# Performance work log

Measured on AMD Instinct MI355X. Metric: run time of the kernel, lower is better.

The kernel has to match this reference:

```python
import jax, jax.numpy as jnp
import numpy as np

D_MODEL = 1024
N_HEADS = 16
HEAD_DIM = D_MODEL // N_HEADS
ROPE_BASE = 10000.0


def setup_inputs() -> dict:
    key = jax.random.key(0)
    ks = jax.random.split(key, 5)
    B, S = 2, 2048
    x = jax.random.normal(ks[0], (B, S, D_MODEL), dtype=jnp.float32)
    scale = 1.0 / np.sqrt(D_MODEL)
    Wq = jax.random.normal(ks[1], (D_MODEL, D_MODEL), dtype=jnp.float32) * scale
    Wk = jax.random.normal(ks[2], (D_MODEL, D_MODEL), dtype=jnp.float32) * scale
    Wv = jax.random.normal(ks[3], (D_MODEL, D_MODEL), dtype=jnp.float32) * scale
    Wo = jax.random.normal(ks[4], (D_MODEL, D_MODEL), dtype=jnp.float32) * scale
    return {"x": x, "Wq": Wq, "Wk": Wk, "Wv": Wv, "Wo": Wo}


def _rope_cos_sin(seq_len, dtype):
    # inv_freq over half the head dim, duplicated (cat[freqs, freqs])
    inv_freq = 1.0 / (ROPE_BASE ** (jnp.arange(0, HEAD_DIM, 2, dtype=jnp.float32) / HEAD_DIM))
    t = jnp.arange(seq_len, dtype=jnp.float32)
    freqs = jnp.outer(t, inv_freq)                 # [S, HD/2]
    emb = jnp.concatenate([freqs, freqs], axis=-1)  # [S, HD]
    return jnp.cos(emb).astype(dtype), jnp.sin(emb).astype(dtype)


def _rotate_half(v):
    v1, v2 = jnp.split(v, 2, axis=-1)
    return jnp.concatenate([-v2, v1], axis=-1)


def reference(x, Wq, Wk, Wv, Wo):
    B, S, _ = x.shape
    # torch Linear: y = x @ W.T  (weights stored [out, in])
    def proj(W):
        y = jnp.einsum('bsd,ed->bse', x, W)
        return y.reshape(B, S, N_HEADS, HEAD_DIM).transpose(0, 2, 1, 3)  # [B,H,S,HD]
    q, k, v = proj(Wq), proj(Wk), proj(Wv)

    cos, sin = _rope_cos_sin(S, x.dtype)  # [S, HD]
    cos = cos[None, None]                 # [1,1,S,HD]
    sin = sin[None, None]
    q = q * cos + _rotate_half(q) * sin
    k = k * cos + _rotate_half(k) * sin

    scale = 1.0 / np.sqrt(HEAD_DIM)
    scores = jnp.einsum('bhqd,bhkd->bhqk', q, k) * scale  # [B,H,S,S]
    causal = jnp.triu(jnp.ones((S, S), dtype=bool), k=1)
    scores = jnp.where(causal, jnp.finfo(scores.dtype).min, scores)
    attn = jax.nn.softmax(scores, axis=-1)
    out = jnp.einsum('bhqk,bhkd->bhqd', attn, v)          # [B,H,S,HD]
    out = out.transpose(0, 2, 1, 3).reshape(B, S, D_MODEL)
    return jnp.einsum('bsd,ed->bse', out, Wo)
```

## Files before the change

### kernel.cpp

```cpp
#include <hip/hip_runtime.h>

typedef unsigned short u16;
typedef __attribute__((ext_vector_type(8))) short short8;
typedef __attribute__((ext_vector_type(4))) float floatx4;

#define D_MODEL 1024
#define NHEADS 16
#define HD 64
#define BATCH 2
#define SEQ 2048
#define MROWS (BATCH * SEQ)

static __device__ __forceinline__ u16 f2bf(float f) {
  unsigned int u = __float_as_uint(f);
  u += 0x7fffu + ((u >> 16) & 1u);
  return (u16)(u >> 16);
}

__global__ void cvt_all(const float* __restrict__ x, const float* __restrict__ wq,
                        const float* __restrict__ wk, const float* __restrict__ wv,
                        const float* __restrict__ wo, u16* __restrict__ xb,
                        u16* __restrict__ wqkvb, u16* __restrict__ wob) {
  const int i = blockIdx.x * 256 + threadIdx.x;
  const int chunk = i >> 18;
  const float* src;
  u16* dst;
  int loc;
  switch (chunk) {
    case 0: case 1: case 2: case 3: src = x;  dst = xb;              loc = i;              break;
    case 4:                          src = wq; dst = wqkvb;           loc = i - (4 << 18); break;
    case 5:                          src = wk; dst = wqkvb + 1048576; loc = i - (5 << 18); break;
    case 6:                          src = wv; dst = wqkvb + 2097152; loc = i - (6 << 18); break;
    default:                         src = wo; dst = wob;             loc = i - (7 << 18); break;
  }
  const float4 v = ((const float4*)src)[loc];
  ushort4 o;
  o.x = f2bf(v.x); o.y = f2bf(v.y); o.z = f2bf(v.z); o.w = f2bf(v.w);
  ((ushort4*)dst)[loc] = o;
}

__global__ __launch_bounds__(256) void gemm_qkv(
    const u16* __restrict__ A, const u16* __restrict__ B,
    u16* __restrict__ qb, u16* __restrict__ kb, u16* __restrict__ vb, int K) {
  __shared__ u16 As[2][128 * 32];
  __shared__ u16 Bs[2][128 * 32];
  const int t = threadIdx.x;
  const int lane = t & 63;
  const int wv = t >> 6;
  const int wr = wv >> 1, wc = wv & 1;
  const int m0 = blockIdx.y * 128, n0 = blockIdx.x * 128;
  const int qd = lane >> 4, lr = lane & 15;
  const int arow = lane >> 2;
  const int acol = (lane & 3) * 8;

  floatx4 acc[4][4];
#pragma unroll
  for (int i = 0; i < 4; ++i)
#pragma unroll
    for (int j = 0; j < 4; ++j) acc[i][j] = (floatx4){0.f, 0.f, 0.f, 0.f};

  for (int kt = 0; kt < K; kt += 64) {
    __syncthreads();
#pragma unroll
    for (int kh = 0; kh < 2; ++kh) {
#pragma unroll
      for (int i = 0; i < 2; ++i) {
        const int seg = wv * 2 + i;
        const u16* ga = &A[(size_t)(m0 + seg * 16 + arow) * K + kt + kh * 32 + acol];
        const u16* gb = &B[(size_t)(n0 + seg * 16 + arow) * K + kt + kh * 32 + acol];
        __builtin_amdgcn_global_load_lds(
            (const __attribute__((address_space(1))) void*)ga,
            (__attribute__((address_space(3))) void*)&As[kh][seg * 512], 16, 0, 0);
        __builtin_amdgcn_global_load_lds(
            (const __attribute__((address_space(1))) void*)gb,
            (__attribute__((address_space(3))) void*)&Bs[kh][seg * 512], 16, 0, 0);
      }
    }
    __syncthreads();

#pragma unroll
    for (int kh = 0; kh < 2; ++kh) {
      short8 af[4], bfr[4];
#pragma unroll
      for (int i = 0; i < 4; ++i)
        af[i] = *(const short8*)&As[kh][(wr * 64 + i * 16 + lr) * 32 + qd * 8];
#pragma unroll
      for (int j = 0; j < 4; ++j)
        bfr[j] = *(const short8*)&Bs[kh][(wc * 64 + j * 16 + lr) * 32 + qd * 8];
#pragma unroll
      for (int i = 0; i < 4; ++i)
#pragma unroll
        for (int j = 0; j < 4; ++j)
          acc[i][j] = __builtin_amdgcn_mfma_f32_16x16x32_bf16(af[i], bfr[j], acc[i][j], 0, 0, 0);
    }
  }

  const int tn = n0 >> 10;
  if (tn == 2) {
#pragma unroll
    for (int i = 0; i < 4; ++i) {
      const int mb = m0 + wr * 64 + i * 16 + qd * 4;
      const int b = mb >> 11, s = mb & 2047;
#pragma unroll
      for (int j = 0; j < 4; ++j) {
        const int nn = (n0 + wc * 64 + j * 16 + lr) & 1023;
        const int h = nn >> 6, d = nn & 63;
        ushort4 o;
        o.x = f2bf(acc[i][j][0]); o.y = f2bf(acc[i][j][1]);
        o.z = f2bf(acc[i][j][2]); o.w = f2bf(acc[i][j][3]);
        *(ushort4*)&vb[((size_t)(b * NHEADS + h) * HD + d) * SEQ + s] = o;
      }
    }
  } else {
    u16* dst = (tn == 0) ? qb : kb;
    const float qs = (tn == 0) ? 0.18033688011112042f : 1.0f;
    const int h = ((n0 & 1023) >> 6) + wc;
    const float inv0 = __builtin_exp2f(-(float)lr * 0.4152410118609203f);
    const float inv1 = __builtin_exp2f(-(float)(lr + 16) * 0.4152410118609203f);
#pragma unroll
    for (int i = 0; i < 4; ++i) {
      const int mb = m0 + wr * 64 + i * 16 + qd * 4;
      const int b = mb >> 11;
      const size_t rowbase = (size_t)(b * NHEADS + h) * SEQ;
#pragma unroll
      for (int r = 0; r < 4; ++r) {
        const int sq = (mb + r) & 2047;
        float s0, c0, s1, c1;
        __sincosf((float)sq * inv0, &s0, &c0);
        __sincosf((float)sq * inv1, &s1, &c1);
#pragma unroll
        for (int j = 0; j < 4; ++j) {
          const float v = acc[i][j][r];
          const float pv = acc[i][j ^ 2][r];
          const float cc = (j & 1) ? c1 : c0;
          const float ss = (j & 1) ? s1 : s0;
          const float res = (v * cc + ((j < 2) ? -pv : pv) * ss) * qs;
          dst[(rowbase + sq) * HD + j * 16 + lr] = f2bf(res);
        }
      }
    }
  }
}

__global__ __launch_bounds__(256) void gemm_out(
    const u16* __restrict__ A, const u16* __restrict__ B, float* __restrict__ fo,
    int N, int K) {
  __shared__ u16 As[2][64 * 32];
  __shared__ u16 Bs[2][64 * 32];
  const int t = threadIdx.x;
  const int lane = t & 63, wv = t >> 6;
  const int m0 = blockIdx.y * 64, n0 = blockIdx.x * 64;
  const int qd = lane >> 4, lr = lane & 15;
  const int arow = lane >> 2;
  const int acol = (lane & 3) * 8;

  floatx4 acc[4];
#pragma unroll
  for (int j = 0; j < 4; ++j) acc[j] = (floatx4){0.f, 0.f, 0.f, 0.f};

  for (int kt = 0; kt < K; kt += 64) {
    __syncthreads();
#pragma unroll
    for (int kh = 0; kh < 2; ++kh) {
      const u16* ga = &A[(size_t)(m0 + wv * 16 + arow) * K + kt + kh * 32 + acol];
      const u16* gb = &B[(size_t)(n0 + wv * 16 + arow) * K + kt + kh * 32 + acol];
      __builtin_amdgcn_global_load_lds(
          (const __attribute__((address_space(1))) void*)ga,
          (__attribute__((address_space(3))) void*)&As[kh][wv * 512], 16, 0, 0);
      __builtin_amdgcn_global_load_lds(
          (const __attribute__((address_space(1))) void*)gb,
          (__attribute__((address_space(3))) void*)&Bs[kh][wv * 512], 16, 0, 0);
    }
    __syncthreads();

#pragma unroll
    for (int kh = 0; kh < 2; ++kh) {
      const short8 af = *(const short8*)&As[kh][(wv * 16 + lr) * 32 + qd * 8];
#pragma unroll
      for (int j = 0; j < 4; ++j) {
        const short8 bfr = *(const short8*)&Bs[kh][(j * 16 + lr) * 32 + qd * 8];
        acc[j] = __builtin_amdgcn_mfma_f32_16x16x32_bf16(af, bfr, acc[j], 0, 0, 0);
      }
    }
  }
#pragma unroll
  for (int j = 0; j < 4; ++j)
#pragma unroll
    for (int r = 0; r < 4; ++r)
      fo[(size_t)(m0 + wv * 16 + qd * 4 + r) * N + n0 + j * 16 + lr] = acc[j][r];
}

__global__ __launch_bounds__(512, 4) void flash_mfma(
    const u16* __restrict__ Q, const u16* __restrict__ Kg,
    const u16* __restrict__ Vg, u16* __restrict__ O) {
  __shared__ u16 Ks[2][2][64 * 32];
  __shared__ u16 Vs[2][2][64 * 32];
  __shared__ u16 Ps[8][16][72];
  const int t = threadIdx.x;
  const int lane = t & 63, wv = t >> 6;
  const int lr = lane & 15, qd = lane >> 4;
  const int bh = blockIdx.x;
  const int y = (int)blockIdx.y;
  const int c = (y < 8) ? (15 - y) : (y - 8);
  const int nsteps = 2 * c + 2;
  const int q0w = c * 128 + wv * 16;
  const size_t baseQK = (size_t)bh * SEQ * HD;
  const size_t baseV = (size_t)bh * HD * SEQ;
  const int b = bh >> 4, h = bh & 15;
  const int srow = lane >> 2;
  const int scol = (lane & 3) * 8;
  const int shh = (wv >> 2) & 1;
  const int sseg = wv & 3;

  auto stage = [&](int buf, int k0) {
    const u16* gk = &Kg[baseQK + (size_t)(k0 + sseg * 16 + srow) * HD + shh * 32 + scol];
    __builtin_amdgcn_global_load_lds(
        (const __attribute__((address_space(1))) void*)gk,
        (__attribute__((address_space(3))) void*)&Ks[buf][shh][sseg * 512], 16, 0, 0);
    const u16* gv = &Vg[baseV + (size_t)(sseg * 16 + srow) * SEQ + k0 + shh * 32 + scol];
    __builtin_amdgcn_global_load_lds(
        (const __attribute__((address_space(1))) void*)gv,
        (__attribute__((address_space(3))) void*)&Vs[buf][shh][sseg * 512], 16, 0, 0);
  };

  short8 qf[2];
#pragma unroll
  for (int s = 0; s < 2; ++s)
    qf[s] = *(const short8*)&Q[baseQK + (size_t)(q0w + lr) * HD + s * 32 + qd * 8];

  float l_i = 0.f;
  floatx4 oacc[4];
#pragma unroll
  for (int dj = 0; dj < 4; ++dj) oacc[dj] = (floatx4){0.f, 0.f, 0.f, 0.f};

  stage(0, 0);

  for (int kt = 0; kt < nsteps; ++kt) {
    __syncthreads();
    if (kt + 1 < nsteps) stage((kt + 1) & 1, (kt + 1) * 64);
    const int k0 = kt * 64;
    if (k0 > q0w + 15) continue;
    const int buf = kt & 1;

    short8 kf[2][4], vf[2][4];
#pragma unroll
    for (int s = 0; s < 2; ++s)
#pragma unroll
      for (int jj = 0; jj < 4; ++jj)
        kf[s][jj] = *(const short8*)&Ks[buf][s][(jj * 16 + lr) * 32 + qd * 8];
#pragma unroll
    for (int s = 0; s < 2; ++s)
#pragma unroll
      for (int dj = 0; dj < 4; ++dj)
        vf[s][dj] = *(const short8*)&Vs[buf][s][(dj * 16 + lr) * 32 + qd * 8];

    floatx4 sv[4];
#pragma unroll
    for (int jj = 0; jj < 4; ++jj) sv[jj] = (floatx4){0.f, 0.f, 0.f, 0.f};
#pragma unroll
    for (int s = 0; s < 2; ++s)
#pragma unroll
      for (int jj = 0; jj < 4; ++jj)
        sv[jj] = __builtin_amdgcn_mfma_f32_16x16x32_bf16(kf[s][jj], qf[s], sv[jj], 0, 0, 0);

    const int dq = q0w - k0;
    if (dq < 63) {
#pragma unroll
      for (int jj = 0; jj < 4; ++jj)
#pragma unroll
        for (int r = 0; r < 4; ++r)
          if (jj * 16 + qd * 4 + r > dq + lr) sv[jj][r] = -1e30f;
    }

    float rs = 0.f;
#pragma unroll
    for (int jj = 0; jj < 4; ++jj) {
      const float p0 = __builtin_exp2f(sv[jj][0]);
      const float p1 = __builtin_exp2f(sv[jj][1]);
      const float p2 = __builtin_exp2f(sv[jj][2]);
      const float p3 = __builtin_exp2f(sv[jj][3]);
      rs += (p0 + p1) + (p2 + p3);
      uint2 pk;
      pk.x = __builtin_amdgcn_perm(__float_as_uint(p1), __float_as_uint(p0), 0x07060302);
      pk.y = __builtin_amdgcn_perm(__float_as_uint(p3), __float_as_uint(p2), 0x07060302);
      *(uint2*)&Ps[wv][lr][jj * 16 + qd * 4] = pk;
    }
    l_i += rs;

    const short8 pf0 = *(const short8*)&Ps[wv][lr][qd * 8];
    const short8 pf1 = *(const short8*)&Ps[wv][lr][32 + qd * 8];
#pragma unroll
    for (int dj = 0; dj < 4; ++dj)
      oacc[dj] = __builtin_amdgcn_mfma_f32_16x16x32_bf16(pf0, vf[0][dj], oacc[dj], 0, 0, 0);
#pragma unroll
    for (int dj = 0; dj < 4; ++dj)
      oacc[dj] = __builtin_amdgcn_mfma_f32_16x16x32_bf16(pf1, vf[1][dj], oacc[dj], 0, 0, 0);
  }

  {
    float lf = l_i;
    lf += __shfl_xor(lf, 16, 64);
    lf += __shfl_xor(lf, 32, 64);
#pragma unroll
    for (int r = 0; r < 4; ++r) {
      const float linv = 1.f / __shfl(lf, qd * 4 + r, 64);
      const int q = q0w + qd * 4 + r;
#pragma unroll
      for (int dj = 0; dj < 4; ++dj)
        O[(size_t)(b * SEQ + q) * D_MODEL + h * HD + dj * 16 + lr] = f2bf(oacc[dj][r] * linv);
    }
  }
}

extern "C" void kernel_launch(void* const* d_in, const int* in_sizes, int n_in,
                              void* d_out, int out_size, void* d_ws, size_t ws_size,
                              hipStream_t stream) {
  const float* x  = (const float*)d_in[0];
  const float* Wq = (const float*)d_in[1];
  const float* Wk = (const float*)d_in[2];
  const float* Wv = (const float*)d_in[3];
  const float* Wo = (const float*)d_in[4];
  float* out = (float*)d_out;

  u16* xb = (u16*)d_ws;
  u16* wqkv = xb + 4194304;
  u16* wo = wqkv + 3145728;
  u16* qb = wo + 1048576;
  u16* kb = qb + 4194304;
  u16* vb = kb + 4194304;
  u16* ow = vb + 4194304;

  cvt_all<<<8192, 256, 0, stream>>>(x, Wq, Wk, Wv, Wo, xb, wqkv, wo);
  gemm_qkv<<<dim3(24, 32), 256, 0, stream>>>(xb, wqkv, qb, kb, vb, 1024);
  flash_mfma<<<dim3(32, 16), 512, 0, stream>>>(qb, kb, vb, ow);
  gemm_out<<<dim3(16, 64), 256, 0, stream>>>(ow, wo, out, 1024, 1024);
}
```

Before: 182.4 us.

## Split flash attention into 32-row query blocks across two parity launches

The attention kernel moves from 512-thread blocks covering 128 query rows to 128-thread blocks covering 32 query rows. The work is split across two launches by query-chunk parity, with a zig-zag mapping to balance the causal workload. K/V staging now goes through one wave each for K and V, and a helper wraps the global-to-LDS load. The intent is finer-grained load balance and more blocks in flight, at the cost of an extra launch, less K/V reuse per block, and more redundant K/V traffic.

```diff
diff --git a/kernel.cpp b/kernel.cpp
--- a/kernel.cpp
+++ b/kernel.cpp
@@ -15,6 +15,12 @@
   unsigned int u = __float_as_uint(f);
   u += 0x7fffu + ((u >> 16) & 1u);
   return (u16)(u >> 16);
+}
+
+static __device__ __forceinline__ void glds16(const u16* g, u16* l) {
+  __builtin_amdgcn_global_load_lds(
+      (const __attribute__((address_space(1))) void*)g,
+      (__attribute__((address_space(3))) void*)l, 16, 0, 0);
 }
 
 __global__ void cvt_all(const float* __restrict__ x, const float* __restrict__ wq,
@@ -66,14 +72,8 @@
 #pragma unroll
       for (int i = 0; i < 2; ++i) {
         const int seg = wv * 2 + i;
-        const u16* ga = &A[(size_t)(m0 + seg * 16 + arow) * K + kt + kh * 32 + acol];
-        const u16* gb = &B[(size_t)(n0 + seg * 16 + arow) * K + kt + kh * 32 + acol];
-        __builtin_amdgcn_global_load_lds(
-            (const __attribute__((address_space(1))) void*)ga,
-            (__attribute__((address_space(3))) void*)&As[kh][seg * 512], 16, 0, 0);
-        __builtin_amdgcn_global_load_lds(
-            (const __attribute__((address_space(1))) void*)gb,
-            (__attribute__((address_space(3))) void*)&Bs[kh][seg * 512], 16, 0, 0);
+        glds16(&A[(size_t)(m0 + seg * 16 + arow) * K + kt + kh * 32 + acol], &As[kh][seg * 512]);
+        glds16(&B[(size_t)(n0 + seg * 16 + arow) * K + kt + kh * 32 + acol], &Bs[kh][seg * 512]);
       }
     }
     __syncthreads();
@@ -162,14 +162,8 @@
     __syncthreads();
 #pragma unroll
     for (int kh = 0; kh < 2; ++kh) {
-      const u16* ga = &A[(size_t)(m0 + wv * 16 + arow) * K + kt + kh * 32 + acol];
-      const u16* gb = &B[(size_t)(n0 + wv * 16 + arow) * K + kt + kh * 32 + acol];
-      __builtin_amdgcn_global_load_lds(
-          (const __attribute__((address_space(1))) void*)ga,
-          (__attribute__((address_space(3))) void*)&As[kh][wv * 512], 16, 0, 0);
-      __builtin_amdgcn_global_load_lds(
-          (const __attribute__((address_space(1))) void*)gb,
-          (__attribute__((address_space(3))) void*)&Bs[kh][wv * 512], 16, 0, 0);
+      glds16(&A[(size_t)(m0 + wv * 16 + arow) * K + kt + kh * 32 + acol], &As[kh][wv * 512]);
+      glds16(&B[(size_t)(n0 + wv * 16 + arow) * K + kt + kh * 32 + acol], &Bs[kh][wv * 512]);
     }
     __syncthreads();
 
@@ -190,37 +184,44 @@
       fo[(size_t)(m0 + wv * 16 + qd * 4 + r) * N + n0 + j * 16 + lr] = acc[j][r];
 }
 
-__global__ __launch_bounds__(512, 4) void flash_mfma(
+__global__ __launch_bounds__(128, 2) void flash_mfma(
     const u16* __restrict__ Q, const u16* __restrict__ Kg,
-    const u16* __restrict__ Vg, u16* __restrict__ O) {
+    const u16* __restrict__ Vg, u16* __restrict__ O, int parity) {
   __shared__ u16 Ks[2][2][64 * 32];
   __shared__ u16 Vs[2][2][64 * 32];
-  __shared__ u16 Ps[8][16][72];
+  __shared__ u16 Ps[2][16][72];
   const int t = threadIdx.x;
   const int lane = t & 63, wv = t >> 6;
   const int lr = lane & 15, qd = lane >> 4;
   const int bh = blockIdx.x;
-  const int y = (int)blockIdx.y;
-  const int c = (y < 8) ? (15 - y) : (y - 8);
-  const int nsteps = 2 * c + 2;
-  const int q0w = c * 128 + wv * 16;
+  const int yy = (int)blockIdx.y;
+  const int qq = yy >> 3, g = yy & 7;
+  const int m = (qq == 0) ? g : (qq == 1) ? (15 - g) : (qq == 2) ? (16 + g) : (31 - g);
+  const int c = 2 * m + parity;
+  const int nst = (c >> 1) + 1;
+  const int q0w = c * 32 + wv * 16;
   const size_t baseQK = (size_t)bh * SEQ * HD;
   const size_t baseV = (size_t)bh * HD * SEQ;
   const int b = bh >> 4, h = bh & 15;
   const int srow = lane >> 2;
   const int scol = (lane & 3) * 8;
-  const int shh = (wv >> 2) & 1;
-  const int sseg = wv & 3;
 
   auto stage = [&](int buf, int k0) {
-    const u16* gk = &Kg[baseQK + (size_t)(k0 + sseg * 16 + srow) * HD + shh * 32 + scol];
-    __builtin_amdgcn_global_load_lds(
-        (const __attribute__((address_space(1))) void*)gk,
-        (__attribute__((address_space(3))) void*)&Ks[buf][shh][sseg * 512], 16, 0, 0);
-    const u16* gv = &Vg[baseV + (size_t)(sseg * 16 + srow) * SEQ + k0 + shh * 32 + scol];
-    __builtin_amdgcn_global_load_lds(
-        (const __attribute__((address_space(1))) void*)gv,
-        (__attribute__((address_space(3))) void*)&Vs[buf][shh][sseg * 512], 16, 0, 0);
+    if (wv == 0) {
+#pragma unroll
+      for (int hh = 0; hh < 2; ++hh)
+#pragma unroll
+        for (int seg = 0; seg < 4; ++seg)
+          glds16(&Kg[baseQK + (size_t)(k0 + seg * 16 + srow) * HD + hh * 32 + scol],
+                 &Ks[buf][hh][seg * 512]);
+    } else {
+#pragma unroll
+      for (int hh = 0; hh < 2; ++hh)
+#pragma unroll
+        for (int seg = 0; seg < 4; ++seg)
+          glds16(&Vg[baseV + (size_t)(seg * 16 + srow) * SEQ + k0 + hh * 32 + scol],
+                 &Vs[buf][hh][seg * 512]);
+    }
   };
 
   short8 qf[2];
@@ -235,9 +236,9 @@
 
   stage(0, 0);
 
-  for (int kt = 0; kt < nsteps; ++kt) {
-    __syncthreads();
-    if (kt + 1 < nsteps) stage((kt + 1) & 1, (kt + 1) * 64);
+  for (int kt = 0; kt < nst; ++kt) {
+    __syncthreads();
+    if (kt + 1 < nst) stage((kt + 1) & 1, (kt + 1) * 64);
     const int k0 = kt * 64;
     if (k0 > q0w + 15) continue;
     const int buf = kt & 1;
@@ -332,6 +333,7 @@
 
   cvt_all<<<8192, 256, 0, stream>>>(x, Wq, Wk, Wv, Wo, xb, wqkv, wo);
   gemm_qkv<<<dim3(24, 32), 256, 0, stream>>>(xb, wqkv, qb, kb, vb, 1024);
-  flash_mfma<<<dim3(32, 16), 512, 0, stream>>>(qb, kb, vb, ow);
+  flash_mfma<<<dim3(32, 32), 128, 0, stream>>>(qb, kb, vb, ow, 1);
+  flash_mfma<<<dim3(32, 32), 128, 0, stream>>>(qb, kb, vb, ow, 0);
   gemm_out<<<dim3(16, 64), 256, 0, stream>>>(ow, wo, out, 1024, 1024);
 }
```

New measurement: 198.0 us. 8.6% more time.
